# Kernel optimization log

Measured on AMD Instinct MI355X. Metric: run time of the kernel, lower is better.

Reference implementation:

```python
import jax, jax.numpy as jnp
import numpy as np

SCALE_FACTOR = 2
KERNEL_SIZE = SCALE_FACTOR + 1  # 3
SIGMA = 2.0
EPS = 1e-6


def _gaussian_kernel(k, sigma, dtype):
    ax = jnp.arange(k, dtype=jnp.float32) - (k - 1) / 2.0
    g = jnp.exp(-(ax[:, None] ** 2 + ax[None, :] ** 2) / (2.0 * sigma ** 2))
    return (g / g.sum()).astype(dtype)


def _smooth(img, kernel):
    # img: [B,H,W,C], kernel: [k,k]; depthwise gaussian blur, SAME padding
    C = img.shape[-1]
    k = kernel.shape[0]
    kern = jnp.tile(kernel[:, :, None, None], (1, 1, 1, C))  # HWIO, I=1 per group
    return jax.lax.conv_general_dilated(
        img, kern, window_strides=(1, 1), padding=[(k // 2, k // 2)] * 2,
        dimension_numbers=('NHWC', 'HWIO', 'NHWC'), feature_group_count=C)


def setup_inputs() -> dict:
    key = jax.random.key(0)
    k1, k2 = jax.random.split(key)
    B, N, C = 8, 3072, 256
    x = jax.random.normal(k1, (B, N, C), dtype=jnp.float32)
    loc = jax.random.uniform(k2, (B, N, 2), dtype=jnp.float32, minval=-1.0, maxval=1.0)
    return {"x": x, "loc": loc, "h": 64, "w": 48}


def reference(x, loc, h, w):
    # token2map(x, loc, [h*sf, w*sf], kernel_size=sf+1, sigma=2)
    H, W = int(h * SCALE_FACTOR), int(w * SCALE_FACTOR)
    B, N, C = x.shape
    loc = jnp.clip(loc, -1.0, 1.0)
    px = 0.5 * (loc[..., 0] + 1.0) * W - 0.5
    py = 0.5 * (loc[..., 1] + 1.0) * H - 0.5
    ix = jnp.clip(jnp.round(px).astype(jnp.int32), 0, W - 1)  # [B,N]
    iy = jnp.clip(jnp.round(py).astype(jnp.int32), 0, H - 1)
    idx = ix + iy * W + jnp.arange(B, dtype=jnp.int32)[:, None] * (H * W)  # [B,N]

    # scatter-add features and counts into the flat grid
    src = jnp.concatenate([x, jnp.ones((B, N, 1), x.dtype)], axis=-1).reshape(B * N, C + 1)
    acc = jnp.zeros((B * H * W, C + 1), x.dtype).at[idx.reshape(-1)].add(src)
    acc = acc.reshape(B, H, W, C + 1)
    feature = acc[..., :C]
    count = acc[..., C:]

    feature = feature / (count + EPS)
    mask = (count > 0).astype(x.dtype)
    feature = feature * mask

    # gaussian interpolation to fill empty cells
    kernel = _gaussian_kernel(KERNEL_SIZE, SIGMA, x.dtype)
    feat_s = _smooth(feature, kernel)
    mask_s = _smooth(mask, kernel)
    feat_s = feat_s / (mask_s + EPS)
    feat_s = feat_s * (mask_s > 0).astype(x.dtype)
    feature = feature + (1.0 - mask) * feat_s

    return jnp.transpose(feature, (0, 3, 1, 2))  # [B,C,H,W] to match torch layout
```

## Files before the change

### kernel.cpp

```cpp
#include <hip/hip_runtime.h>

#define B_  8
#define N_  3072
#define C_  256
#define H_  128
#define W_  96
#define HW_ (H_ * W_)
#define NC_ (B_ * HW_)
#define NT_ (B_ * N_)
#define EPSF 1e-6f

#define KW0 0.13080118f
#define KW1 0.11543166f
#define KW2 0.10186807f

#define CG_ 64
#define XT_ 32
#define XS_ 34
#define CPB 72

#define OFF_ASTART 0
#define OFF_ACUR   (NC_ + 1)
#define OFF_BSUM   (2 * NC_ + 1)
#define OFF_BOFF   (2 * NC_ + 1 + 384)
#define OFF_TOKS   (2 * NC_ + 1 + 768)

__device__ __forceinline__ unsigned short f2bf(float f) {
    const unsigned u = __float_as_uint(f);
    return (unsigned short)((u + 0x7FFFu + ((u >> 16) & 1u)) >> 16);
}

__device__ __forceinline__ void token_cell(const float* __restrict__ loc, int token,
                                           int& b, int& ix, int& iy) {
    b = token / N_;
    const float lx = fminf(fmaxf(loc[2 * token + 0], -1.0f), 1.0f);
    const float ly = fminf(fmaxf(loc[2 * token + 1], -1.0f), 1.0f);
    const float px = 0.5f * (lx + 1.0f) * (float)W_ - 0.5f;
    const float py = 0.5f * (ly + 1.0f) * (float)H_ - 0.5f;
    ix = (int)rintf(px); ix = min(max(ix, 0), W_ - 1);
    iy = (int)rintf(py); iy = min(max(iy, 0), H_ - 1);
}

__global__ void count_k(const float* __restrict__ loc, unsigned* __restrict__ cnts) {
    const int token = blockIdx.x * 256 + threadIdx.x;
    int b, ix, iy;
    token_cell(loc, token, b, ix, iy);
    atomicAdd(&cnts[b * HW_ + iy * W_ + ix], 1u);
}

__global__ void scanA(const unsigned* __restrict__ cnts, unsigned* __restrict__ Bsum) {
    const int i = blockIdx.x * 256 + threadIdx.x;
    int c = (int)cnts[i];
    #pragma unroll
    for (int off = 32; off > 0; off >>= 1) c += __shfl_down(c, off, 64);
    __shared__ int s[4];
    if ((threadIdx.x & 63) == 0) s[threadIdx.x >> 6] = c;
    __syncthreads();
    if (threadIdx.x == 0) Bsum[blockIdx.x] = (unsigned)(s[0] + s[1] + s[2] + s[3]);
}

__global__ void scanB(const unsigned* __restrict__ Bsum, unsigned* __restrict__ Boff) {
    __shared__ unsigned s[512];
    const int t = threadIdx.x;
    const unsigned v = (t < 384) ? Bsum[t] : 0u;
    s[t] = v;
    __syncthreads();
    #pragma unroll
    for (int off = 1; off < 512; off <<= 1) {
        const unsigned a = (t >= off) ? s[t - off] : 0u;
        __syncthreads();
        s[t] += a;
        __syncthreads();
    }
    if (t < 384) Boff[t] = s[t] - v;
}

__global__ void scanC(const unsigned* __restrict__ Boff,
                      unsigned* __restrict__ Astart, unsigned* __restrict__ Acur) {
    __shared__ unsigned s[256];
    const int t = threadIdx.x;
    const int i = blockIdx.x * 256 + t;
    const unsigned v = Acur[i];
    s[t] = v;
    __syncthreads();
    #pragma unroll
    for (int off = 1; off < 256; off <<= 1) {
        const unsigned a = (t >= off) ? s[t - off] : 0u;
        __syncthreads();
        s[t] += a;
        __syncthreads();
    }
    const unsigned excl = s[t] - v + Boff[blockIdx.x];
    Astart[i] = excl;
    Acur[i]   = excl;
    if (i == 0) Astart[NC_] = NT_;
}

__global__ void fill_bins(const float* __restrict__ loc,
                          unsigned* __restrict__ Acur, unsigned* __restrict__ toks) {
    const int token = blockIdx.x * 256 + threadIdx.x;
    int b, ix, iy;
    token_cell(loc, token, b, ix, iy);
    const unsigned pos = atomicAdd(&Acur[b * HW_ + iy * W_ + ix], 1u);
    toks[pos] = ((unsigned)ix << 20) | (unsigned)token;
}

__device__ __forceinline__ void gather_row(const float* __restrict__ xf,
        const unsigned* __restrict__ Astart, const unsigned* __restrict__ toks,
        unsigned short* __restrict__ Ms, unsigned* __restrict__ Fs,
        int b, int yg, int xs, int cg, int lane) {
    const int cellbase = b * HW_ + yg * W_;
    unsigned a = 0u;
    if (lane < XS_ + 1) {
        int g = xs - 1 + lane;
        g = min(max(g, 0), W_);
        a = Astart[cellbase + g];
    }
    const unsigned an = __shfl_down(a, 1, 64);
    if (lane < XS_) Fs[lane] = an - a;
    const unsigned p0 = __shfl(a, 0, 64);
    const unsigned p1 = __shfl(a, XS_, 64);

    int cur_xi = -1;
    float acc = 0.0f;
    unsigned cnt = 0u;
    for (unsigned p = p0; p < p1; p += 4) {
        unsigned vv[4]; float ff[4];
        #pragma unroll
        for (int j = 0; j < 4; ++j)
            if (p + j < p1) vv[j] = toks[p + j];
        #pragma unroll
        for (int j = 0; j < 4; ++j)
            if (p + j < p1)
                ff[j] = xf[(size_t)(vv[j] & 0xFFFFFu) * C_ + cg * CG_ + lane];
        #pragma unroll
        for (int j = 0; j < 4; ++j) {
            if (p + j >= p1) break;
            const int xi = (int)(vv[j] >> 20) - xs + 1;
            if (xi != cur_xi) {
                if (cur_xi >= 0)
                    Ms[cur_xi * CPB + lane] = f2bf(acc / ((float)cnt + EPSF));
                acc = 0.0f; cnt = 0u; cur_xi = xi;
            }
            acc += ff[j]; ++cnt;
        }
    }
    if (cur_xi >= 0)
        Ms[cur_xi * CPB + lane] = f2bf(acc / ((float)cnt + EPSF));
}

__device__ __forceinline__ void bf4_to_f32(const unsigned short* p, float* f) {
    const uint2 v = *(const uint2*)p;
    f[0] = __uint_as_float(v.x << 16);
    f[1] = __uint_as_float(v.x & 0xFFFF0000u);
    f[2] = __uint_as_float(v.y << 16);
    f[3] = __uint_as_float(v.y & 0xFFFF0000u);
}

__global__ __launch_bounds__(256) void fused_k(const float* __restrict__ xf,
        const unsigned* __restrict__ Astart, const unsigned* __restrict__ toks,
        float* __restrict__ out) {
    const int blk = blockIdx.x;
    const int cg = blk & 3;
    const int t2 = blk >> 2;
    const int xt = t2 % 3;
    const int t3 = t2 / 3;
    const int y  = t3 & 127;
    const int b  = t3 >> 7;
    const int xs = xt * XT_;
    const int lane = threadIdx.x & 63;
    const int wv = threadIdx.x >> 6;

    __shared__ __align__(16) unsigned short means[3 * XS_ * CPB];
    __shared__ unsigned cflag[3][XS_];

    {
        uint4* p4 = (uint4*)means;
        #pragma unroll
        for (int i = threadIdx.x; i < 3 * XS_ * CPB / 8; i += 256)
            p4[i] = make_uint4(0u, 0u, 0u, 0u);
    }
    __syncthreads();

    if (wv < 3) {
        const int yg = y - 1 + wv;
        if ((unsigned)yg < (unsigned)H_)
            gather_row(xf, Astart, toks, means + wv * XS_ * CPB, cflag[wv],
                       b, yg, xs, cg, lane);
        else if (lane < XS_) cflag[wv][lane] = 0u;
    }
    __syncthreads();

    const int xl  = threadIdx.x & 31;
    const int sub = threadIdx.x >> 5;
    const int xi  = xl + 1;
    const int c0  = sub * 8;
    const unsigned short* M0 = means;
    const unsigned short* M1 = means + XS_ * CPB;
    const unsigned short* M2 = means + 2 * XS_ * CPB;
    float* op = out + ((size_t)(b * C_ + cg * CG_ + c0)) * HW_
                    + (size_t)y * W_ + xs + xl;

    if (cflag[1][xi] != 0u) {
        #pragma unroll
        for (int q = 0; q < 2; ++q) {
            float m[4];
            bf4_to_f32(&M1[xi * CPB + c0 + q * 4], m);
            op[(size_t)(q * 4 + 0) * HW_] = m[0];
            op[(size_t)(q * 4 + 1) * HW_] = m[1];
            op[(size_t)(q * 4 + 2) * HW_] = m[2];
            op[(size_t)(q * 4 + 3) * HW_] = m[3];
        }
    } else {
        const float w00 = cflag[0][xi - 1] ? KW2 : 0.0f;
        const float w01 = cflag[0][xi]     ? KW1 : 0.0f;
        const float w02 = cflag[0][xi + 1] ? KW2 : 0.0f;
        const float w10 = cflag[1][xi - 1] ? KW1 : 0.0f;
        const float w12 = cflag[1][xi + 1] ? KW1 : 0.0f;
        const float w20 = cflag[2][xi - 1] ? KW2 : 0.0f;
        const float w21 = cflag[2][xi]     ? KW1 : 0.0f;
        const float w22 = cflag[2][xi + 1] ? KW2 : 0.0f;
        const float ms = ((w00 + w02) + (w20 + w22)) + ((w01 + w21) + (w10 + w12));
        const float inv = 1.0f / (ms + EPSF);
        #pragma unroll
        for (int q = 0; q < 2; ++q) {
            const int cq = c0 + q * 4;
            const int im = (xi - 1) * CPB + cq;
            const int ic = (xi    ) * CPB + cq;
            const int ip = (xi + 1) * CPB + cq;
            float a0[4], a1[4], a2[4], b0[4], b2[4], d0[4], d1[4], d2[4];
            bf4_to_f32(&M0[im], a0); bf4_to_f32(&M0[ic], a1); bf4_to_f32(&M0[ip], a2);
            bf4_to_f32(&M1[im], b0);                          bf4_to_f32(&M1[ip], b2);
            bf4_to_f32(&M2[im], d0); bf4_to_f32(&M2[ic], d1); bf4_to_f32(&M2[ip], d2);
            #pragma unroll
            for (int k = 0; k < 4; ++k) {
                const float fs = w00*a0[k] + w01*a1[k] + w02*a2[k]
                               + w10*b0[k] + w12*b2[k]
                               + w20*d0[k] + w21*d1[k] + w22*d2[k];
                op[(size_t)(q * 4 + k) * HW_] = fs * inv;
            }
        }
    }
}

extern "C" void kernel_launch(void* const* d_in, const int* in_sizes, int n_in,
                              void* d_out, int out_size, void* d_ws, size_t ws_size,
                              hipStream_t stream) {
    const float* x   = (const float*)d_in[0];
    const float* loc = (const float*)d_in[1];
    float* out = (float*)d_out;

    unsigned* W32 = (unsigned*)d_ws;
    unsigned* Astart = W32 + OFF_ASTART;
    unsigned* Acur   = W32 + OFF_ACUR;
    unsigned* Bsum   = W32 + OFF_BSUM;
    unsigned* Boff   = W32 + OFF_BOFF;
    unsigned* toks   = W32 + OFF_TOKS;

    hipMemsetAsync(Acur, 0, (size_t)NC_ * sizeof(unsigned), stream);

    count_k  <<<NT_ / 256, 256, 0, stream>>>(loc, Acur);
    scanA    <<<NC_ / 256, 256, 0, stream>>>(Acur, Bsum);
    scanB    <<<1, 512, 0, stream>>>(Bsum, Boff);
    scanC    <<<NC_ / 256, 256, 0, stream>>>(Boff, Astart, Acur);
    fill_bins<<<NT_ / 256, 256, 0, stream>>>(loc, Acur, toks);

    fused_k<<<B_ * H_ * 3 * 4, 256, 0, stream>>>(x, Astart, toks, out);
}
```

Before: 67.31 us.

## Widen channel group to 128 with float2 gathers and ballot occupancy masks

Each block now handles 128 channels instead of 64. Each lane gathers a float2 and writes packed bf16 pairs, so the per-row token list and Astart scan are traversed half as often across channel groups. Per-cell occupancy flags are replaced by a 64-bit ballot mask per row. The trade-off is half as many blocks, a larger shared tile, and 16 channels per thread in the output stage, which lowers parallelism and raises register use.

```diff
diff --git a/kernel.cpp b/kernel.cpp
--- a/kernel.cpp
+++ b/kernel.cpp
@@ -14,10 +14,10 @@
 #define KW1 0.11543166f
 #define KW2 0.10186807f
 
-#define CG_ 64
+#define CG_ 128
 #define XT_ 32
 #define XS_ 34
-#define CPB 72
+#define CPB 132
 
 #define OFF_ASTART 0
 #define OFF_ACUR   (NC_ + 1)
@@ -25,9 +25,9 @@
 #define OFF_BOFF   (2 * NC_ + 1 + 384)
 #define OFF_TOKS   (2 * NC_ + 1 + 768)
 
-__device__ __forceinline__ unsigned short f2bf(float f) {
+__device__ __forceinline__ unsigned f2bf(float f) {
     const unsigned u = __float_as_uint(f);
-    return (unsigned short)((u + 0x7FFFu + ((u >> 16) & 1u)) >> 16);
+    return (u + 0x7FFFu + ((u >> 16) & 1u)) >> 16;
 }
 
 __device__ __forceinline__ void token_cell(const float* __restrict__ loc, int token,
@@ -107,7 +107,7 @@
 
 __device__ __forceinline__ void gather_row(const float* __restrict__ xf,
         const unsigned* __restrict__ Astart, const unsigned* __restrict__ toks,
-        unsigned short* __restrict__ Ms, unsigned* __restrict__ Fs,
+        unsigned short* __restrict__ Ms, unsigned long long* __restrict__ cm,
         int b, int yg, int xs, int cg, int lane) {
     const int cellbase = b * HW_ + yg * W_;
     unsigned a = 0u;
@@ -117,36 +117,44 @@
         a = Astart[cellbase + g];
     }
     const unsigned an = __shfl_down(a, 1, 64);
-    if (lane < XS_) Fs[lane] = an - a;
+    const unsigned long long mask = __ballot(lane < XS_ && an > a);
+    if (lane == 0) *cm = mask;
     const unsigned p0 = __shfl(a, 0, 64);
     const unsigned p1 = __shfl(a, XS_, 64);
 
+    unsigned* msw = (unsigned*)Ms;
     int cur_xi = -1;
-    float acc = 0.0f;
+    float acc0 = 0.0f, acc1 = 0.0f;
     unsigned cnt = 0u;
     for (unsigned p = p0; p < p1; p += 4) {
-        unsigned vv[4]; float ff[4];
+        unsigned vv[4]; float2 ff[4];
         #pragma unroll
         for (int j = 0; j < 4; ++j)
             if (p + j < p1) vv[j] = toks[p + j];
         #pragma unroll
         for (int j = 0; j < 4; ++j)
             if (p + j < p1)
-                ff[j] = xf[(size_t)(vv[j] & 0xFFFFFu) * C_ + cg * CG_ + lane];
+                ff[j] = *(const float2*)&xf[(size_t)(vv[j] & 0xFFFFFu) * C_
+                                            + cg * CG_ + 2 * lane];
         #pragma unroll
         for (int j = 0; j < 4; ++j) {
             if (p + j >= p1) break;
             const int xi = (int)(vv[j] >> 20) - xs + 1;
             if (xi != cur_xi) {
-                if (cur_xi >= 0)
-                    Ms[cur_xi * CPB + lane] = f2bf(acc / ((float)cnt + EPSF));
-                acc = 0.0f; cnt = 0u; cur_xi = xi;
+                if (cur_xi >= 0) {
+                    const float rcp = 1.0f / ((float)cnt + EPSF);
+                    msw[cur_xi * (CPB / 2) + lane] =
+                        f2bf(acc0 * rcp) | (f2bf(acc1 * rcp) << 16);
+                }
+                acc0 = acc1 = 0.0f; cnt = 0u; cur_xi = xi;
             }
-            acc += ff[j]; ++cnt;
+            acc0 += ff[j].x; acc1 += ff[j].y; ++cnt;
         }
     }
-    if (cur_xi >= 0)
-        Ms[cur_xi * CPB + lane] = f2bf(acc / ((float)cnt + EPSF));
+    if (cur_xi >= 0) {
+        const float rcp = 1.0f / ((float)cnt + EPSF);
+        msw[cur_xi * (CPB / 2) + lane] = f2bf(acc0 * rcp) | (f2bf(acc1 * rcp) << 16);
+    }
 }
 
 __device__ __forceinline__ void bf4_to_f32(const unsigned short* p, float* f) {
@@ -161,8 +169,8 @@
         const unsigned* __restrict__ Astart, const unsigned* __restrict__ toks,
         float* __restrict__ out) {
     const int blk = blockIdx.x;
-    const int cg = blk & 3;
-    const int t2 = blk >> 2;
+    const int cg = blk & 1;
+    const int t2 = blk >> 1;
     const int xt = t2 % 3;
     const int t3 = t2 / 3;
     const int y  = t3 & 127;
@@ -172,11 +180,10 @@
     const int wv = threadIdx.x >> 6;
 
     __shared__ __align__(16) unsigned short means[3 * XS_ * CPB];
-    __shared__ unsigned cflag[3][XS_];
+    __shared__ unsigned long long cmask[3];
 
     {
         uint4* p4 = (uint4*)means;
-        #pragma unroll
         for (int i = threadIdx.x; i < 3 * XS_ * CPB / 8; i += 256)
             p4[i] = make_uint4(0u, 0u, 0u, 0u);
     }
@@ -185,45 +192,45 @@
     if (wv < 3) {
         const int yg = y - 1 + wv;
         if ((unsigned)yg < (unsigned)H_)
-            gather_row(xf, Astart, toks, means + wv * XS_ * CPB, cflag[wv],
+            gather_row(xf, Astart, toks, means + wv * XS_ * CPB, &cmask[wv],
                        b, yg, xs, cg, lane);
-        else if (lane < XS_) cflag[wv][lane] = 0u;
+        else if (lane == 0) cmask[wv] = 0ULL;
     }
     __syncthreads();
 
     const int xl  = threadIdx.x & 31;
     const int sub = threadIdx.x >> 5;
     const int xi  = xl + 1;
-    const int c0  = sub * 8;
+    const int c0  = sub * 16;
+    const unsigned long long cm0 = cmask[0], cm1 = cmask[1], cm2 = cmask[2];
     const unsigned short* M0 = means;
     const unsigned short* M1 = means + XS_ * CPB;
     const unsigned short* M2 = means + 2 * XS_ * CPB;
     float* op = out + ((size_t)(b * C_ + cg * CG_ + c0)) * HW_
                     + (size_t)y * W_ + xs + xl;
 
-    if (cflag[1][xi] != 0u) {
-        #pragma unroll
-        for (int q = 0; q < 2; ++q) {
+    if ((cm1 >> xi) & 1ULL) {
+        #pragma unroll
+        for (int q = 0; q < 4; ++q) {
             float m[4];
             bf4_to_f32(&M1[xi * CPB + c0 + q * 4], m);
-            op[(size_t)(q * 4 + 0) * HW_] = m[0];
-            op[(size_t)(q * 4 + 1) * HW_] = m[1];
-            op[(size_t)(q * 4 + 2) * HW_] = m[2];
-            op[(size_t)(q * 4 + 3) * HW_] = m[3];
+            #pragma unroll
+            for (int k = 0; k < 4; ++k)
+                op[(size_t)(q * 4 + k) * HW_] = m[k];
         }
     } else {
-        const float w00 = cflag[0][xi - 1] ? KW2 : 0.0f;
-        const float w01 = cflag[0][xi]     ? KW1 : 0.0f;
-        const float w02 = cflag[0][xi + 1] ? KW2 : 0.0f;
-        const float w10 = cflag[1][xi - 1] ? KW1 : 0.0f;
-        const float w12 = cflag[1][xi + 1] ? KW1 : 0.0f;
-        const float w20 = cflag[2][xi - 1] ? KW2 : 0.0f;
-        const float w21 = cflag[2][xi]     ? KW1 : 0.0f;
-        const float w22 = cflag[2][xi + 1] ? KW2 : 0.0f;
+        const float w00 = ((cm0 >> (xi - 1)) & 1ULL) ? KW2 : 0.0f;
+        const float w01 = ((cm0 >> xi)       & 1ULL) ? KW1 : 0.0f;
+        const float w02 = ((cm0 >> (xi + 1)) & 1ULL) ? KW2 : 0.0f;
+        const float w10 = ((cm1 >> (xi - 1)) & 1ULL) ? KW1 : 0.0f;
+        const float w12 = ((cm1 >> (xi + 1)) & 1ULL) ? KW1 : 0.0f;
+        const float w20 = ((cm2 >> (xi - 1)) & 1ULL) ? KW2 : 0.0f;
+        const float w21 = ((cm2 >> xi)       & 1ULL) ? KW1 : 0.0f;
+        const float w22 = ((cm2 >> (xi + 1)) & 1ULL) ? KW2 : 0.0f;
         const float ms = ((w00 + w02) + (w20 + w22)) + ((w01 + w21) + (w10 + w12));
         const float inv = 1.0f / (ms + EPSF);
         #pragma unroll
-        for (int q = 0; q < 2; ++q) {
+        for (int q = 0; q < 4; ++q) {
             const int cq = c0 + q * 4;
             const int im = (xi - 1) * CPB + cq;
             const int ic = (xi    ) * CPB + cq;
@@ -265,5 +272,5 @@
     scanC    <<<NC_ / 256, 256, 0, stream>>>(Boff, Astart, Acur);
     fill_bins<<<NT_ / 256, 256, 0, stream>>>(loc, Acur, toks);
 
-    fused_k<<<B_ * H_ * 3 * 4, 256, 0, stream>>>(x, Astart, toks, out);
-}
+    fused_k<<<B_ * H_ * 3 * 2, 256, 0, stream>>>(x, Astart, toks, out);
+}
```

Result: no change. 67.38 us (+0.1%).
